# Kernel optimization log

Hardware: AMD Instinct MI355X
Metric: run time of the kernel (lower is better)

Reference implementation:

```python
import jax, jax.numpy as jnp
import numpy as np

N_HEAD = 16
HEAD_DIM = 64
N_EMBD = N_HEAD * HEAD_DIM  # 1024


def setup_inputs() -> dict:
    key = jax.random.key(0)
    ks = jax.random.split(key, 5)
    B, S = 2, 2048
    x = jax.random.normal(ks[0], (B, S, N_EMBD), dtype=jnp.float32)
    qkv_w = jax.random.normal(ks[1], (N_EMBD, 3 * N_EMBD), dtype=jnp.float32) * 0.02
    qkv_b = jax.random.normal(ks[2], (3 * N_EMBD,), dtype=jnp.float32) * 0.02
    proj_w = jax.random.normal(ks[3], (N_EMBD, N_EMBD), dtype=jnp.float32) * 0.02
    proj_b = jax.random.normal(ks[4], (N_EMBD,), dtype=jnp.float32) * 0.02
    return {"x": x, "qkv_w": qkv_w, "qkv_b": qkv_b, "proj_w": proj_w, "proj_b": proj_b}


def reference(x, qkv_w, qkv_b, proj_w, proj_b):
    B, S, _ = x.shape
    qkv = x @ qkv_w + qkv_b  # [B,S,3E]
    q, k, v = jnp.split(qkv, 3, axis=-1)
    # [B,H,S,D]
    q = q.reshape(B, S, N_HEAD, HEAD_DIM).transpose(0, 2, 1, 3)
    k = k.reshape(B, S, N_HEAD, HEAD_DIM).transpose(0, 2, 1, 3)
    v = v.reshape(B, S, N_HEAD, HEAD_DIM).transpose(0, 2, 1, 3)
    scale = 1.0 / jnp.sqrt(jnp.float32(HEAD_DIM))
    scores = jnp.einsum('bhqd,bhkd->bhqk', q, k) * scale  # [B,H,S,S]
    causal = jnp.tril(jnp.ones((S, S), dtype=bool))
    scores = jnp.where(causal[None, None], scores, jnp.float32(-jnp.inf))
    attn = jax.nn.softmax(scores, axis=-1)  # dropout p=0 (eval)
    out = jnp.einsum('bhqk,bhkd->bhqd', attn, v)
    out = out.transpose(0, 2, 1, 3).reshape(B, S, N_EMBD)
    out = out @ proj_w + proj_b  # resid dropout p=0
    return out, k, v
```

## Files before the change

### kernel.cpp

```cpp
#include <hip/hip_runtime.h>
#include <hip/hip_bf16.h>


typedef __attribute__((ext_vector_type(4))) float f32x4;
typedef __attribute__((ext_vector_type(16))) float f32x16;
typedef __attribute__((ext_vector_type(8))) short s16x8;
typedef __attribute__((ext_vector_type(4))) short s16x4;

__device__ __forceinline__ short f2bf(float f) {
    union { float f; unsigned u; } x{f};
    unsigned r = x.u + 0x7fff + ((x.u >> 16) & 1);
    return (short)(r >> 16);
}

__device__ __forceinline__ void gload_lds16(const void* g, void* l) {
    __builtin_amdgcn_global_load_lds(
        (const __attribute__((address_space(1))) void*)g,
        (__attribute__((address_space(3))) void*)l, 16, 0, 0);
}

__global__ __launch_bounds__(256) void fused_prepass(const float* __restrict__ x,
                                                     short* __restrict__ x_bf,
                                                     const float* __restrict__ qkv_w,
                                                     short* __restrict__ wT1,
                                                     const float* __restrict__ proj_w,
                                                     short* __restrict__ wT2) {
    __shared__ float tile[32][33];
    const int bid = blockIdx.x, tid = threadIdx.x;
    if (bid < 2048) {
        int i = (bid * 256 + tid) * 8;
        f32x4 a = *(const f32x4*)&x[i];
        f32x4 b = *(const f32x4*)&x[i + 4];
        s16x8 o;
        #pragma unroll
        for (int j = 0; j < 4; ++j) o[j] = f2bf(a[j]);
        #pragma unroll
        for (int j = 0; j < 4; ++j) o[j + 4] = f2bf(b[j]);
        *(s16x8*)&x_bf[i] = o;
        return;
    }
    const float* in;
    short* out;
    int K = 1024, N, n0, k0;
    if (bid < 5120) {
        int blk = bid - 2048;
        in = qkv_w; out = wT1; N = 3072;
        n0 = (blk % 96) * 32; k0 = (blk / 96) * 32;
    } else {
        int blk = bid - 5120;
        in = proj_w; out = wT2; N = 1024;
        n0 = (blk & 31) * 32; k0 = (blk >> 5) * 32;
    }
    const int tx = tid & 31, ty = tid >> 5;
    #pragma unroll
    for (int r = 0; r < 4; ++r)
        tile[ty + r * 8][tx] = in[(long)(k0 + ty + r * 8) * N + n0 + tx];
    __syncthreads();
    #pragma unroll
    for (int r = 0; r < 4; ++r)
        out[(long)(n0 + ty + r * 8) * K + k0 + tx] = f2bf(tile[tx][ty + r * 8]);
}

template <int MODE>
__global__ __launch_bounds__(256) void gemm_bf16(
    const short* __restrict__ A, const short* __restrict__ Bt,
    const float* __restrict__ bias, int M, int N, int K,
    float* __restrict__ outf,
    short* __restrict__ qbf, short* __restrict__ kbf, short* __restrict__ vbfT,
    float* __restrict__ kout, float* __restrict__ vout) {
    __shared__ __align__(16) short As[128 * 64];
    __shared__ __align__(16) short Bs[128 * 64];
    const int tid = threadIdx.x;
    const int l = tid & 63, w = tid >> 6;
    const int lr = l >> 4, lc = l & 15;
    const int wm = w >> 1, wn = w & 1;
    const int bid = blockIdx.x;
    const int xcd = bid & 7, s = bid >> 3;
    int bx, by;
    if (MODE == 1) { bx = (xcd & 1) * 12 + s % 12; by = (xcd >> 1) * 8 + s / 12; }
    else           { bx = (xcd & 1) * 4 + (s & 3); by = (xcd >> 1) * 8 + (s >> 2); }
    const int m0 = by * 128, n0 = bx * 128;

    f32x4 acc[4][4] = {};

    for (int kb = 0; kb < K; kb += 64) {
        __syncthreads();
        #pragma unroll
        for (int j = 0; j < 4; ++j) {
            const int c = tid + 256 * j;
            const int row = c >> 3;
            const int lseg = (c & 7) ^ (row & 7);
            gload_lds16(A + (long)(m0 + row) * K + kb + lseg * 8, As + c * 8);
            gload_lds16(Bt + (long)(n0 + row) * K + kb + lseg * 8, Bs + c * 8);
        }
        __syncthreads();
        #pragma unroll
        for (int kh = 0; kh < 2; ++kh) {
            s16x8 af[4], bfr[4];
            #pragma unroll
            for (int mi = 0; mi < 4; ++mi) {
                const int row = wm * 64 + mi * 16 + lc;
                af[mi] = *(const s16x8*)&As[row * 64 + (((kh * 4 + lr) ^ (lc & 7)) * 8)];
            }
            #pragma unroll
            for (int ni = 0; ni < 4; ++ni) {
                const int row = wn * 64 + ni * 16 + lc;
                bfr[ni] = *(const s16x8*)&Bs[row * 64 + (((kh * 4 + lr) ^ (lc & 7)) * 8)];
            }
            #pragma unroll
            for (int mi = 0; mi < 4; ++mi)
                #pragma unroll
                for (int ni = 0; ni < 4; ++ni)
                    acc[mi][ni] = __builtin_amdgcn_mfma_f32_16x16x32_bf16(
                        af[mi], bfr[ni], acc[mi][ni], 0, 0, 0);
        }
    }

    #pragma unroll
    for (int mi = 0; mi < 4; ++mi) {
        #pragma unroll
        for (int ni = 0; ni < 4; ++ni) {
            int col = n0 + wn * 64 + ni * 16 + lc;
            float bv = bias[col];
            if (MODE == 1) {
                int sec = col >> 10, rem = col & 1023;
                int h = rem >> 6, d = rem & 63;
                int row0 = m0 + wm * 64 + mi * 16 + lr * 4;
                int b = row0 >> 11, s0 = row0 & 2047;
                long idxSD = ((long)((b << 4) + h) * 2048 + s0) * 64 + d;
                if (sec == 0) {
                    #pragma unroll
                    for (int i = 0; i < 4; ++i) {
                        float val = acc[mi][ni][i] + bv;
                        qbf[idxSD + (long)i * 64] = f2bf(val * 0.1803368801111244f);
                    }
                } else if (sec == 1) {
                    #pragma unroll
                    for (int i = 0; i < 4; ++i) {
                        float val = acc[mi][ni][i] + bv;
                        kout[idxSD + (long)i * 64] = val;
                        kbf[idxSD + (long)i * 64] = f2bf(val);
                    }
                } else {
                    s16x4 pk;
                    #pragma unroll
                    for (int i = 0; i < 4; ++i) {
                        float val = acc[mi][ni][i] + bv;
                        vout[idxSD + (long)i * 64] = val;
                        pk[i] = f2bf(val);
                    }
                    *(s16x4*)&vbfT[((long)((b << 4) + h) * 64 + d) * 2048 + s0] = pk;
                }
            } else {
                #pragma unroll
                for (int i = 0; i < 4; ++i) {
                    int row = m0 + wm * 64 + mi * 16 + lr * 4 + i;
                    outf[(long)row * N + col] = acc[mi][ni][i] + bv;
                }
            }
        }
    }
}

__global__ __launch_bounds__(256, 2) void attn_kernel(const short* __restrict__ qbf,
                                                      const short* __restrict__ kbf,
                                                      const short* __restrict__ vbfT,
                                                      short* __restrict__ obf) {
    const int bid = blockIdx.x;
    const int xcd = bid & 7, r = bid >> 3;
    const int head_local = r & 3, q16 = r >> 2;
    const int qt = (q16 < 8) ? (q16 + 8) : (15 - q16);
    const int bh = xcd * 4 + head_local;
    const int tid = threadIdx.x;
    const int wv = tid >> 6, l = tid & 63;
    const int h = l >> 5;
    const int l8 = l & 7;
    const int q0 = qt * 128 + wv * 32;
    const int qlane = q0 + (l & 31);
    const long baseSD = (long)bh * 2048 * 64;
    const long baseDS = (long)bh * 64 * 2048;

    __shared__ __align__(16) short Ks[2][64 * 64];
    __shared__ __align__(16) short Vs[2][64 * 64];

    const int sSub = l >> 3;
    const int sChunk = (l & 7) ^ sSub;
    auto stage = [&](int kt, int nb) {
        const int k0 = kt * 64;
        const int r0 = wv * 16 + sSub;
        gload_lds16(kbf + baseSD + (long)(k0 + r0) * 64 + sChunk * 8,
                    &Ks[nb][(wv * 16) * 64]);
        gload_lds16(kbf + baseSD + (long)(k0 + r0 + 8) * 64 + sChunk * 8,
                    &Ks[nb][(wv * 16 + 8) * 64]);
        gload_lds16(vbfT + baseDS + (long)r0 * 2048 + k0 + sChunk * 8,
                    &Vs[nb][(wv * 16) * 64]);
        gload_lds16(vbfT + baseDS + (long)(r0 + 8) * 2048 + k0 + sChunk * 8,
                    &Vs[nb][(wv * 16 + 8) * 64]);
    };

    s16x8 qf[4];
    #pragma unroll
    for (int dd = 0; dd < 4; ++dd)
        qf[dd] = *(const s16x8*)&qbf[baseSD + (long)qlane * 64 + dd * 16 + h * 8];

    f32x4 lacc = {};
    f32x16 O[2] = {};

    const int nkt = 2 * qt + 2;

    stage(0, 0);
    __syncthreads();
    int cur = 0;

    for (int kt = 0; kt < nkt; ++kt) {
        const int k0 = kt * 64;
        if (kt + 1 < nkt) stage(kt + 1, cur ^ 1);

        if (k0 <= q0 + 31) {
            const short* Kb = Ks[cur];
            const short* Vb = Vs[cur];
            #pragma unroll
            for (int kk2 = 0; kk2 < 2; ++kk2) {
                f32x16 z = {};
                #pragma unroll
                for (int dd = 0; dd < 4; ++dd) {
                    s16x8 kf = *(const s16x8*)&Kb[(kk2 * 32 + (l & 31)) * 64 +
                                                  (((2 * dd + h) ^ l8) * 8)];
                    z = __builtin_amdgcn_mfma_f32_32x32x16_bf16(kf, qf[dd], z, 0, 0, 0);
                }
                if (k0 + 63 > q0) {
                    #pragma unroll
                    for (int rr = 0; rr < 16; ++rr) {
                        int kpos = k0 + kk2 * 32 + (rr & 3) + 8 * (rr >> 2) + 4 * h;
                        if (kpos > qlane) z[rr] = -INFINITY;
                    }
                }
                float p[16];
                #pragma unroll
                for (int rr = 0; rr < 16; ++rr) {
                    p[rr] = __builtin_amdgcn_exp2f(z[rr]);
                    lacc[rr & 3] += p[rr];
                }
                #pragma unroll
                for (int f = 0; f < 2; ++f) {
                    union { __hip_bfloat162 b2[4]; s16x8 v; } pk;
                    #pragma unroll
                    for (int j = 0; j < 4; ++j)
                        pk.b2[j] = __float22bfloat162_rn(
                            make_float2(p[f * 8 + 2 * j], p[f * 8 + 2 * j + 1]));
                    const int c0 = kk2 * 4 + f * 2;
                    #pragma unroll
                    for (int dt2 = 0; dt2 < 2; ++dt2) {
                        const short* vr = &Vb[(dt2 * 32 + (l & 31)) * 64];
                        s16x8 vf;
                        *(s16x4*)&vf = *(const s16x4*)&vr[(c0 ^ l8) * 8 + 4 * h];
                        *(((s16x4*)&vf) + 1) = *(const s16x4*)&vr[((c0 + 1) ^ l8) * 8 + 4 * h];
                        O[dt2] = __builtin_amdgcn_mfma_f32_32x32x16_bf16(vf, pk.v,
                                                                         O[dt2], 0, 0, 0);
                    }
                }
            }
        }
        __syncthreads();
        cur ^= 1;
    }

    float lsum = (lacc[0] + lacc[1]) + (lacc[2] + lacc[3]);
    lsum += __shfl_xor(lsum, 32);
    const int b = bh >> 4, hd = bh & 15;
    float inv = 1.0f / lsum;
    #pragma unroll
    for (int dt2 = 0; dt2 < 2; ++dt2) {
        #pragma unroll
        for (int g = 0; g < 4; ++g) {
            s16x4 o;
            #pragma unroll
            for (int i = 0; i < 4; ++i) o[i] = f2bf(O[dt2][g * 4 + i] * inv);
            const int d = dt2 * 32 + 8 * g + 4 * h;
            *(s16x4*)&obf[(long)(b * 2048 + qlane) * 1024 + hd * 64 + d] = o;
        }
    }
}


extern "C" void kernel_launch(void* const* d_in, const int* in_sizes, int n_in,
                              void* d_out, int out_size, void* d_ws, size_t ws_size,
                              hipStream_t stream) {
    const float* x = (const float*)d_in[0];
    const float* qkv_w = (const float*)d_in[1];
    const float* qkv_b = (const float*)d_in[2];
    const float* proj_w = (const float*)d_in[3];
    const float* proj_b = (const float*)d_in[4];

    float* out = (float*)d_out;
    float* kout = out + 4194304;
    float* vout = out + 8388608;

    short* x_bf = (short*)d_ws;
    short* wT1 = x_bf + 4194304;
    short* wT2 = wT1 + 3145728;
    short* q_bf = wT2 + 1048576;
    short* k_bf = q_bf + 4194304;
    short* vT_bf = k_bf + 4194304;
    short* o_bf = x_bf;

    fused_prepass<<<6144, 256, 0, stream>>>(x, x_bf, qkv_w, wT1, proj_w, wT2);

    gemm_bf16<1><<<768, 256, 0, stream>>>(x_bf, wT1, qkv_b, 4096, 3072, 1024,
                                          nullptr, q_bf, k_bf, vT_bf, kout, vout);

    attn_kernel<<<512, 256, 0, stream>>>(q_bf, k_bf, vT_bf, o_bf);

    gemm_bf16<2><<<256, 256, 0, stream>>>(o_bf, wT2, proj_b, 4096, 1024, 1024,
                                          out, nullptr, nullptr, nullptr, nullptr, nullptr);
}
```

Baseline: 109.7 us.

## Split attention key tiles across two wave groups and merge partial outputs in LDS

The attention block grows from 256 to 512 threads. Two groups of four waves each take one 32-key half of every 64-key tile, so per-wave MFMA chain length halves and more waves are resident to hide latency. After the loop, the second group writes its partial O and row sums to a new LDS buffer, and the first group adds them in before normalising and storing. The cost is extra LDS (about 36KB for the merge buffer), a final barrier, and higher register pressure from the 512-thread, 4-blocks-per-CU launch bound.

```diff
diff --git a/kernel.cpp b/kernel.cpp
--- a/kernel.cpp
+++ b/kernel.cpp
@@ -162,7 +162,7 @@
     }
 }
 
-__global__ __launch_bounds__(256, 2) void attn_kernel(const short* __restrict__ qbf,
+__global__ __launch_bounds__(512, 4) void attn_kernel(const short* __restrict__ qbf,
                                                       const short* __restrict__ kbf,
                                                       const short* __restrict__ vbfT,
                                                       short* __restrict__ obf) {
@@ -173,29 +173,27 @@
     const int bh = xcd * 4 + head_local;
     const int tid = threadIdx.x;
     const int wv = tid >> 6, l = tid & 63;
+    const int strip = wv & 3, kh = wv >> 2;
     const int h = l >> 5;
     const int l8 = l & 7;
-    const int q0 = qt * 128 + wv * 32;
+    const int q0 = qt * 128 + strip * 32;
     const int qlane = q0 + (l & 31);
     const long baseSD = (long)bh * 2048 * 64;
     const long baseDS = (long)bh * 64 * 2048;
 
     __shared__ __align__(16) short Ks[2][64 * 64];
     __shared__ __align__(16) short Vs[2][64 * 64];
+    __shared__ __align__(16) float MG[4][64][36];
 
     const int sSub = l >> 3;
     const int sChunk = (l & 7) ^ sSub;
     auto stage = [&](int kt, int nb) {
         const int k0 = kt * 64;
-        const int r0 = wv * 16 + sSub;
+        const int r0 = wv * 8 + sSub;
         gload_lds16(kbf + baseSD + (long)(k0 + r0) * 64 + sChunk * 8,
-                    &Ks[nb][(wv * 16) * 64]);
-        gload_lds16(kbf + baseSD + (long)(k0 + r0 + 8) * 64 + sChunk * 8,
-                    &Ks[nb][(wv * 16 + 8) * 64]);
+                    &Ks[nb][(wv * 8) * 64]);
         gload_lds16(vbfT + baseDS + (long)r0 * 2048 + k0 + sChunk * 8,
-                    &Vs[nb][(wv * 16) * 64]);
-        gload_lds16(vbfT + baseDS + (long)(r0 + 8) * 2048 + k0 + sChunk * 8,
-                    &Vs[nb][(wv * 16 + 8) * 64]);
+                    &Vs[nb][(wv * 8) * 64]);
     };
 
     s16x8 qf[4];
@@ -213,51 +211,48 @@
     int cur = 0;
 
     for (int kt = 0; kt < nkt; ++kt) {
-        const int k0 = kt * 64;
         if (kt + 1 < nkt) stage(kt + 1, cur ^ 1);
-
-        if (k0 <= q0 + 31) {
+        const int kbase = kt * 64 + kh * 32;
+
+        if (kbase <= q0 + 31) {
             const short* Kb = Ks[cur];
             const short* Vb = Vs[cur];
-            #pragma unroll
-            for (int kk2 = 0; kk2 < 2; ++kk2) {
-                f32x16 z = {};
-                #pragma unroll
-                for (int dd = 0; dd < 4; ++dd) {
-                    s16x8 kf = *(const s16x8*)&Kb[(kk2 * 32 + (l & 31)) * 64 +
-                                                  (((2 * dd + h) ^ l8) * 8)];
-                    z = __builtin_amdgcn_mfma_f32_32x32x16_bf16(kf, qf[dd], z, 0, 0, 0);
+            f32x16 z = {};
+            #pragma unroll
+            for (int dd = 0; dd < 4; ++dd) {
+                s16x8 kf = *(const s16x8*)&Kb[(kh * 32 + (l & 31)) * 64 +
+                                              (((2 * dd + h) ^ l8) * 8)];
+                z = __builtin_amdgcn_mfma_f32_32x32x16_bf16(kf, qf[dd], z, 0, 0, 0);
+            }
+            if (kbase + 31 > q0) {
+                #pragma unroll
+                for (int rr = 0; rr < 16; ++rr) {
+                    int kpos = kbase + (rr & 3) + 8 * (rr >> 2) + 4 * h;
+                    if (kpos > qlane) z[rr] = -INFINITY;
                 }
-                if (k0 + 63 > q0) {
-                    #pragma unroll
-                    for (int rr = 0; rr < 16; ++rr) {
-                        int kpos = k0 + kk2 * 32 + (rr & 3) + 8 * (rr >> 2) + 4 * h;
-                        if (kpos > qlane) z[rr] = -INFINITY;
-                    }
-                }
-                float p[16];
-                #pragma unroll
-                for (int rr = 0; rr < 16; ++rr) {
-                    p[rr] = __builtin_amdgcn_exp2f(z[rr]);
-                    lacc[rr & 3] += p[rr];
-                }
-                #pragma unroll
-                for (int f = 0; f < 2; ++f) {
-                    union { __hip_bfloat162 b2[4]; s16x8 v; } pk;
-                    #pragma unroll
-                    for (int j = 0; j < 4; ++j)
-                        pk.b2[j] = __float22bfloat162_rn(
-                            make_float2(p[f * 8 + 2 * j], p[f * 8 + 2 * j + 1]));
-                    const int c0 = kk2 * 4 + f * 2;
-                    #pragma unroll
-                    for (int dt2 = 0; dt2 < 2; ++dt2) {
-                        const short* vr = &Vb[(dt2 * 32 + (l & 31)) * 64];
-                        s16x8 vf;
-                        *(s16x4*)&vf = *(const s16x4*)&vr[(c0 ^ l8) * 8 + 4 * h];
-                        *(((s16x4*)&vf) + 1) = *(const s16x4*)&vr[((c0 + 1) ^ l8) * 8 + 4 * h];
-                        O[dt2] = __builtin_amdgcn_mfma_f32_32x32x16_bf16(vf, pk.v,
-                                                                         O[dt2], 0, 0, 0);
-                    }
+            }
+            float p[16];
+            #pragma unroll
+            for (int rr = 0; rr < 16; ++rr) {
+                p[rr] = __builtin_amdgcn_exp2f(z[rr]);
+                lacc[rr & 3] += p[rr];
+            }
+            #pragma unroll
+            for (int f = 0; f < 2; ++f) {
+                union { __hip_bfloat162 b2[4]; s16x8 v; } pk;
+                #pragma unroll
+                for (int j = 0; j < 4; ++j)
+                    pk.b2[j] = __float22bfloat162_rn(
+                        make_float2(p[f * 8 + 2 * j], p[f * 8 + 2 * j + 1]));
+                const int c0 = kh * 4 + f * 2;
+                #pragma unroll
+                for (int dt2 = 0; dt2 < 2; ++dt2) {
+                    const short* vr = &Vb[(dt2 * 32 + (l & 31)) * 64];
+                    s16x8 vf;
+                    *(s16x4*)&vf = *(const s16x4*)&vr[(c0 ^ l8) * 8 + 4 * h];
+                    *(((s16x4*)&vf) + 1) = *(const s16x4*)&vr[((c0 + 1) ^ l8) * 8 + 4 * h];
+                    O[dt2] = __builtin_amdgcn_mfma_f32_32x32x16_bf16(vf, pk.v,
+                                                                     O[dt2], 0, 0, 0);
                 }
             }
         }
@@ -266,18 +261,33 @@
     }
 
     float lsum = (lacc[0] + lacc[1]) + (lacc[2] + lacc[3]);
-    lsum += __shfl_xor(lsum, 32);
-    const int b = bh >> 4, hd = bh & 15;
-    float inv = 1.0f / lsum;
-    #pragma unroll
-    for (int dt2 = 0; dt2 < 2; ++dt2) {
-        #pragma unroll
-        for (int g = 0; g < 4; ++g) {
-            s16x4 o;
-            #pragma unroll
-            for (int i = 0; i < 4; ++i) o[i] = f2bf(O[dt2][g * 4 + i] * inv);
-            const int d = dt2 * 32 + 8 * g + 4 * h;
-            *(s16x4*)&obf[(long)(b * 2048 + qlane) * 1024 + hd * 64 + d] = o;
+    if (kh == 1) {
+        float* row = &MG[strip][l][0];
+        #pragma unroll
+        for (int dt2 = 0; dt2 < 2; ++dt2)
+            #pragma unroll
+            for (int rr = 0; rr < 16; ++rr)
+                row[dt2 * 16 + rr] = O[dt2][rr];
+        row[32] = lsum;
+    }
+    __syncthreads();
+    if (kh == 0) {
+        const float* row = &MG[strip][l][0];
+        lsum += row[32];
+        lsum += __shfl_xor(lsum, 32);
+        const int b = bh >> 4, hd = bh & 15;
+        float inv = 1.0f / lsum;
+        #pragma unroll
+        for (int dt2 = 0; dt2 < 2; ++dt2) {
+            #pragma unroll
+            for (int g = 0; g < 4; ++g) {
+                s16x4 o;
+                #pragma unroll
+                for (int i = 0; i < 4; ++i)
+                    o[i] = f2bf((O[dt2][g * 4 + i] + row[dt2 * 16 + g * 4 + i]) * inv);
+                const int d = dt2 * 32 + 8 * g + 4 * h;
+                *(s16x4*)&obf[(long)(b * 2048 + qlane) * 1024 + hd * 64 + d] = o;
+            }
         }
     }
 }
@@ -309,7 +319,7 @@
     gemm_bf16<1><<<768, 256, 0, stream>>>(x_bf, wT1, qkv_b, 4096, 3072, 1024,
                                           nullptr, q_bf, k_bf, vT_bf, kout, vout);
 
-    attn_kernel<<<512, 256, 0, stream>>>(q_bf, k_bf, vT_bf, o_bf);
+    attn_kernel<<<512, 512, 0, stream>>>(q_bf, k_bf, vT_bf, o_bf);
 
     gemm_bf16<2><<<256, 256, 0, stream>>>(o_bf, wT2, proj_b, 4096, 1024, 1024,
                                           out, nullptr, nullptr, nullptr, nullptr, nullptr);
```

Measured after the change: 104.5 us. 1.05x faster.
